# Optimization experiments

Measured on AMD Instinct MI355X. Metric: run time of the kernel, lower is better.

The kernel has to match this reference:

```python
import math
import jax, jax.numpy as jnp
import numpy as np

# ---------------- static structure (mirrors CG_woFilter_cuda + MyBatchNormWeightMM) ----------------
LMAX = 4
TAUS = [16, 16, 16, 16, 16]          # t_F: input channels per degree l
T_O  = [16, 16, 16, 16, 16]          # output channels per degree l after weight matmul
BN_EPS = 1e-5

# all (l, l1, l2) triples with l2 <= l1 <= lmax and |l1-l2| <= l <= min(l1+l2, lmax), sorted by (l,l1,l2)
TRIPLES = sorted([(l, l1, l2)
                  for l1 in range(LMAX + 1)
                  for l2 in range(l1 + 1)
                  for l in range(l1 - l2, min(l1 + l2, LMAX) + 1)])

T_FF = [0] * (LMAX + 1)              # t_FF[l] = sum over triples of taus[l1]*taus[l2]
for (l, l1, l2) in TRIPLES:
    T_FF[l] += TAUS[l1] * TAUS[l2]

def _cg_coef(j1, m1, j2, m2, j, m):
    """Clebsch-Gordan coefficient <j1 m1 j2 m2 | j m> (Condon-Shortley)."""
    if m1 + m2 != m:
        return 0.0
    f = math.factorial
    if j < abs(j1 - j2) or j > j1 + j2:
        return 0.0
    pref = math.sqrt((2 * j + 1) * f(j + j1 - j2) * f(j - j1 + j2) * f(j1 + j2 - j) / f(j1 + j2 + j + 1))
    pref *= math.sqrt(f(j + m) * f(j - m) * f(j1 - m1) * f(j1 + m1) * f(j2 - m2) * f(j2 + m2))
    s = 0.0
    for k in range(0, j1 + j2 - j + 1):
        if (j1 - m1 - k) < 0 or (j2 + m2 - k) < 0 or (j - j2 + m1 + k) < 0 or (j - j1 - m2 + k) < 0:
            continue
        s += ((-1.0) ** k) / (f(k) * f(j1 + j2 - j - k) * f(j1 - m1 - k)
                              * f(j2 + m2 - k) * f(j - j2 + m1 + k) * f(j - j1 - m2 + k))
    return pref * s

def _cg_matrix(l, l1, l2):
    C = np.zeros((2 * l + 1, 2 * l1 + 1, 2 * l2 + 1), dtype=np.float32)
    for m in range(-l, l + 1):
        for m1 in range(-l1, l1 + 1):
            m2 = m - m1
            if -l2 <= m2 <= l2:
                C[m + l, m1 + l1, m2 + l2] = _cg_coef(l1, m1, l2, m2, l, m)
    return C

CG_MATS = {t: jnp.asarray(_cg_matrix(*t)) for t in TRIPLES}

M_IN = sum(TAUS[l] * (2 * l + 1) for l in range(LMAX + 1))      # 400
W_LEN = sum(T_FF[l] * T_O[l] for l in range(LMAX + 1))          # 172032


def setup_inputs() -> dict:
    key = jax.random.key(0)
    k1, k2 = jax.random.split(key)
    B = 256
    Fs = jax.random.normal(k1, (B, M_IN, 2), dtype=jnp.float32)
    W = jax.random.normal(k2, (W_LEN, 2), dtype=jnp.float32) * 0.05
    return {"Fs": Fs, "W": W}


def reference(Fs, W):
    B = Fs.shape[0]
    # split input into per-degree blocks: F_l [B, tau, 2l+1, 2]
    Fl, off = [], 0
    for l in range(LMAX + 1):
        n = TAUS[l] * (2 * l + 1)
        Fl.append(Fs[:, off:off + n, :].reshape(B, TAUS[l], 2 * l + 1, 2))
        off += n
    # sparse CG tensor product: per-triple complex outer product contracted with CG coefs
    frags = [[] for _ in range(LMAX + 1)]
    for (l, l1, l2) in TRIPLES:
        C = CG_MATS[(l, l1, l2)]                     # [2l+1, 2l1+1, 2l2+1]
        a, b = Fl[l1], Fl[l2]
        ar, ai = a[..., 0], a[..., 1]
        br, bi = b[..., 0], b[..., 1]
        rr = jnp.einsum('bip,bjq,mpq->bijm', ar, br, C)
        ii = jnp.einsum('bip,bjq,mpq->bijm', ai, bi, C)
        ri = jnp.einsum('bip,bjq,mpq->bijm', ar, bi, C)
        ir = jnp.einsum('bip,bjq,mpq->bijm', ai, br, C)
        fr = (rr - ii).reshape(B, -1, 2 * l + 1)     # channels flattened as c1*tau2 + c2 (t_offsets order)
        fi = (ri + ir).reshape(B, -1, 2 * l + 1)
        frags[l].append(jnp.stack([fr, fi], axis=-1))
    # per-degree fragment batchnorm + complex weight matmul (FN_WMM)
    outs, woff = [], 0
    for l in range(LMAX + 1):
        FF = jnp.concatenate(frags[l], axis=1)       # [B, t_FF, 2l+1, 2]
        var = jnp.mean(jnp.sum(FF * FF, axis=-1), axis=(0, 2))      # per-channel mean |z|^2
        FFn = FF / (jnp.sqrt(var)[None, :, None, None] + BN_EPS)
        n = T_FF[l] * T_O[l]
        Wl = W[woff:woff + n].reshape(T_O[l], T_FF[l], 2)
        woff += n
        wr, wi = Wl[..., 0], Wl[..., 1]
        xr, xi = FFn[..., 0], FFn[..., 1]
        yr = jnp.einsum('oc,bcm->bom', wr, xr) - jnp.einsum('oc,bcm->bom', wi, xi)
        yi = jnp.einsum('oc,bcm->bom', wr, xi) + jnp.einsum('oc,bcm->bom', wi, xr)
        outs.append(jnp.stack([yr, yi], axis=-1).reshape(B, T_O[l] * (2 * l + 1), 2))
    return jnp.concatenate(outs, axis=1)             # [B, sum t_O[l]*(2l+1), 2] = [B, 400, 2]
```

## Files before the change

### kernel.cpp

```cpp
#include <hip/hip_runtime.h>
#include <math.h>

#define NTRI 42
#define NCH  10752
#define B_SZ 256
#define AH_PL 172032

typedef float    f32x4 __attribute__((ext_vector_type(4)));
typedef _Float16 half8 __attribute__((ext_vector_type(8)));
typedef _Float16 f16x2 __attribute__((ext_vector_type(2)));

constexpr int CT_L [NTRI]={0,0,0,0,0, 1,1,1,1,1,1,1,1, 2,2,2,2,2,2,2,2,2,2, 3,3,3,3,3,3,3,3,3,3, 4,4,4,4,4,4,4,4,4};
constexpr int CT_L1[NTRI]={0,1,2,3,4, 1,1,2,2,3,3,4,4, 1,2,2,2,3,3,3,4,4,4, 2,2,3,3,3,3,4,4,4,4, 2,3,3,3,4,4,4,4,4};
constexpr int CT_L2[NTRI]={0,1,2,3,4, 0,1,1,2,2,3,3,4, 1,0,1,2,1,2,3,2,3,4, 1,2,0,1,2,3,1,2,3,4, 2,1,2,3,0,1,2,3,4};
constexpr int CT_T [NTRI]={0,1,2,3,4, 0,1,2,3,4,5,6,7, 0,1,2,3,4,5,6,7,8,9, 0,1,2,3,4,5,6,7,8,9, 0,1,2,3,4,5,6,7,8};

constexpr int KL_t[5]    ={1280,2048,2560,2560,2304};
constexpr int GBASE_t[5] ={0,1280,3328,5888,8448};
constexpr int ROFF_t[5]  ={0,16,64,144,256};
constexpr int NM_t[5]    ={1,3,5,7,9};
constexpr int FFB_t[5]   ={0,327680,1900544,5177344,9764864};
#define FF_TOT 15073280
constexpr int PL_t[5]    ={0,5,29,79,149};
#define PART_PL 4096
#define PART_TOT (230*PART_PL)

__device__ const int   dCTL[NTRI]={0,0,0,0,0, 1,1,1,1,1,1,1,1, 2,2,2,2,2,2,2,2,2,2, 3,3,3,3,3,3,3,3,3,3, 4,4,4,4,4,4,4,4,4};
__device__ const int   dCTT[NTRI]={0,1,2,3,4, 0,1,2,3,4,5,6,7, 0,1,2,3,4,5,6,7,8,9, 0,1,2,3,4,5,6,7,8,9, 0,1,2,3,4,5,6,7,8};
__device__ const int   dK[5]   ={1280,2048,2560,2560,2304};
__device__ const int   dWOFF[5]={0,20480,53248,94208,135168};
__device__ const int   dNM[5]  ={1,3,5,7,9};
__device__ const int   dFFB[5] ={0,327680,1900544,5177344,9764864};
__device__ const int   dPL[5]  ={0,5,29,79,149};
__device__ const int   dGB[5]  ={0,1280,3328,5888,8448};
__device__ const int   dROFF[5]={0,16,64,144,256};
__device__ const int   dNT[5]  ={5,8,10,10,9};
__device__ const float dINV[5] ={1.f/256.f,1.f/768.f,1.f/1280.f,1.f/1792.f,1.f/2304.f};

__device__ float  g_vpart[64*NCH];
__device__ __align__(16) f16x2  g_ff[FF_TOT];
__device__ __align__(16) f16x2  g_ah[2*AH_PL];
__device__ float2 g_part[PART_TOT];

constexpr double cfact(int n){ double r=1.0; for(int i=2;i<=n;i++) r*=(double)i; return r; }
constexpr double csqrt_(double v){ double x = v>1.0? v:1.0; for(int i=0;i<80;i++) x = 0.5*(x+v/x); return x; }
constexpr double ccg(int j1,int m1,int j2,int m2,int j,int m){
    if(m1+m2!=m) return 0.0;
    double pref = csqrt_((2.0*j+1.0)*cfact(j+j1-j2)*cfact(j-j1+j2)*cfact(j1+j2-j)/cfact(j1+j2+j+1));
    pref *= csqrt_(cfact(j+m)*cfact(j-m)*cfact(j1-m1)*cfact(j1+m1)*cfact(j2-m2)*cfact(j2+m2));
    double s=0.0;
    for(int k=0;k<=j1+j2-j;k++){
        int a=j1-m1-k, bb=j2+m2-k, c=j-j2+m1+k, d=j-j1-m2+k;
        if(a<0||bb<0||c<0||d<0) continue;
        double term = 1.0/(cfact(k)*cfact(j1+j2-j-k)*cfact(a)*cfact(bb)*cfact(c)*cfact(d));
        s += (k&1)? -term : term;
    }
    return pref*s;
}
struct CG81 { float a[81]; };
constexpr CG81 makecg(int l,int l1,int l2){
    CG81 t{};
    const int n1=2*l1+1;
    for(int mi=0;mi<2*l+1;mi++)
        for(int p=0;p<n1;p++){
            const int m=mi-l, m1=p-l1, m2=m-m1;
            if(m2>=-l2 && m2<=l2) t.a[mi*n1+p]=(float)ccg(l1,m1,l2,m2,l,m);
        }
    return t;
}
template<int TR> struct CGC { static constexpr CG81 t = makecg(CT_L[TR],CT_L1[TR],CT_L2[TR]); };

template<int TR>
__device__ __forceinline__ void cg_compute_lds(const float2* __restrict__ sF,
                                               int i, int j, float2* __restrict__ ff){
    constexpr int L=CT_L[TR], L1=CT_L1[TR], L2=CT_L2[TR];
    constexpr int N1=2*L1+1, N2=2*L2+1, NM=2*L+1;
    float2 A[N1], Bv[N2];
    #pragma unroll
    for(int p=0;p<N1;p++) A[p]=sF[ROFF_t[L1]+i*N1+p];
    #pragma unroll
    for(int q=0;q<N2;q++) Bv[q]=sF[ROFF_t[L2]+j*N2+q];
    #pragma unroll
    for(int mi=0;mi<NM;mi++){
        float aR=0.f, aI=0.f;
        const int pLo = (mi-L+L1-L2) > 0 ? (mi-L+L1-L2) : 0;
        const int pHi = (mi-L+L1+L2) < 2*L1 ? (mi-L+L1+L2) : 2*L1;
        #pragma unroll
        for(int p=0;p<N1;p++){
            if(p>=pLo && p<=pHi){
                const float c = CGC<TR>::t.a[mi*N1+p];
                if(c != 0.f){
                    const int q = mi - L - p + L1 + L2;
                    const float2 a=A[p], b=Bv[q];
                    aR = fmaf(c, a.x*b.x - a.y*b.y, aR);
                    aI = fmaf(c, a.x*b.y + a.y*b.x, aI);
                }
            }
        }
        ff[mi]=make_float2(aR,aI);
    }
}

template<int TR>
__device__ __forceinline__ void cg_one(const float2* __restrict__ sF, int bc, int t){
    constexpr int L=CT_L[TR], NM=2*L+1, T=CT_T[TR], K=KL_t[L];
    constexpr int NMK=NM*K;
    const int i=t>>4, j=t&15;
    float n2=0.f;
    #pragma unroll
    for(int b4=0;b4<4;b4++){
        const int b=bc*4+b4;
        float2 ff[NM];
        cg_compute_lds<TR>(sF + b4*400, i, j, ff);
        const int base = FFB_t[L] + b*NMK + T*256 + t;
        #pragma unroll
        for(int m=0;m<NM;m++){
            n2 = fmaf(ff[m].x,ff[m].x,n2);
            n2 = fmaf(ff[m].y,ff[m].y,n2);
            f16x2 h; h.x=(_Float16)ff[m].x; h.y=(_Float16)ff[m].y;
            g_ff[base + m*K] = h;
        }
    }
    g_vpart[bc*NCH + GBASE_t[L] + T*256 + t] = n2;
}

template<int TR>
__device__ __forceinline__ void cg_disp(int tr, const float2* sF, int bc, int t){
    if constexpr (TR < NTRI){
        if(tr==TR) cg_one<TR>(sF,bc,t);
        else       cg_disp<TR+1>(tr,sF,bc,t);
    }
}

__global__ void __launch_bounds__(256) k_cg(const float2* __restrict__ Fs){
    __shared__ float4 sF4[800];
    const int bc=blockIdx.y, t=threadIdx.x;
    const float4* __restrict__ F4 = reinterpret_cast<const float4*>(Fs) + bc*800;
    sF4[t]      = F4[t];
    sF4[t+256]  = F4[t+256];
    sF4[t+512]  = F4[t+512];
    if(t<32) sF4[t+768] = F4[t+768];
    __syncthreads();
    cg_disp<0>(blockIdx.x, reinterpret_cast<const float2*>(sF4), bc, t);
}

__global__ void __launch_bounds__(256) k_wn(const float2* __restrict__ W2){
    const int tr=blockIdx.x, t=threadIdx.x;
    const int l=dCTL[tr], T=dCTT[tr], K=dK[l];
    const int ch = dGB[l] + T*256 + t;
    float s=0.f;
    #pragma unroll 8
    for(int bc=0;bc<64;bc++) s += g_vpart[bc*NCH + ch];
    const float invv = 1.f/(sqrtf(s*dINV[l])+1e-5f);
    const int base = dWOFF[l] + T*256 + t;
    #pragma unroll 4
    for(int o=0;o<16;o++){
        const float2 w = W2[base + o*K];
        f16x2 hr, hi;
        hr.x=(_Float16)( w.x*invv); hr.y=(_Float16)(-w.y*invv);
        hi.x=(_Float16)( w.y*invv); hi.y=(_Float16)( w.x*invv);
        g_ah[base + o*K]         = hr;
        g_ah[AH_PL + base + o*K] = hi;
    }
}

__global__ void __launch_bounds__(256) k_mm(){
    const int j=blockIdx.x;
    const int wv=threadIdx.x>>6, lane=threadIdx.x&63;
    const int bg=blockIdx.y*4+wv;
    const int l=(j<5)?0:(j<29)?1:(j<79)?2:(j<149)?3:4;
    const int nm=dNM[l];
    const int loc=j-dPL[l];
    const int T=loc/nm, m=loc-T*nm;
    const int K=dK[l];
    const int l15=lane&15, kg=lane>>4;
    const half8* __restrict__ Arp = reinterpret_cast<const half8*>(g_ah + dWOFF[l] + l15*K + T*256 + kg*4);
    const half8* __restrict__ Aip = reinterpret_cast<const half8*>(g_ah + AH_PL + dWOFF[l] + l15*K + T*256 + kg*4);
    const half8* __restrict__ Xp  = reinterpret_cast<const half8*>(g_ff + dFFB[l] + (bg*16+l15)*(nm*K) + m*K + T*256 + kg*4);
    f32x4 ar0={0.f,0.f,0.f,0.f}, ar1={0.f,0.f,0.f,0.f};
    f32x4 ai0={0.f,0.f,0.f,0.f}, ai1={0.f,0.f,0.f,0.f};
    #pragma unroll
    for(int ks=0; ks<16; ks++){
        const half8 Ar = Arp[ks*4];
        const half8 Ai = Aip[ks*4];
        const half8 Bf = Xp [ks*4];
        if(ks & 1){
            ar1 = __builtin_amdgcn_mfma_f32_16x16x32_f16(Ar, Bf, ar1, 0,0,0);
            ai1 = __builtin_amdgcn_mfma_f32_16x16x32_f16(Ai, Bf, ai1, 0,0,0);
        } else {
            ar0 = __builtin_amdgcn_mfma_f32_16x16x32_f16(Ar, Bf, ar0, 0,0,0);
            ai0 = __builtin_amdgcn_mfma_f32_16x16x32_f16(Ai, Bf, ai0, 0,0,0);
        }
    }
    const f32x4 ar = ar0 + ar1, ai = ai0 + ai1;
    float2* __restrict__ pp = g_part + j*PART_PL + bg*256;
    #pragma unroll
    for(int r=0;r<4;r++){
        pp[(kg*4+r)*16 + l15] = make_float2(ar[r], ai[r]);
    }
}

__global__ void __launch_bounds__(448) k_red(float2* __restrict__ out){
    const int b=blockIdx.x, r=threadIdx.x;
    if(r>=400) return;
    const int l = (r<16)?0:(r<64)?1:(r<144)?2:(r<256)?3:4;
    const int om = r - dROFF[l];
    const int nm = dNM[l];
    const int o = om/nm, m = om - o*nm;
    const float2* __restrict__ pp = g_part + (dPL[l]+m)*PART_PL + (b>>4)*256 + o*16 + (b&15);
    float2 s=make_float2(0.f,0.f);
    const int nt=dNT[l];
    for(int T=0;T<nt;T++){
        const float2 v = pp[T*nm*PART_PL];
        s.x+=v.x; s.y+=v.y;
    }
    out[b*400+r]=s;
}

extern "C" void kernel_launch(void* const* d_in, const int* in_sizes, int n_in,
                              void* d_out, int out_size, void* d_ws, size_t ws_size,
                              hipStream_t stream){
    const float2* Fs = (const float2*)d_in[0];
    const float2* W  = (const float2*)d_in[1];
    float2* out = (float2*)d_out;

    k_cg <<<dim3(NTRI,64), 256, 0, stream>>>(Fs);
    k_wn <<<dim3(NTRI),    256, 0, stream>>>(W);
    k_mm <<<dim3(230,4),   256, 0, stream>>>();
    k_red<<<dim3(B_SZ),    448, 0, stream>>>(out);
}
```

Before: 120.8 us.

## Pair channels per thread in CG, atomically reduce variance, double batch tiles in MFMA

The CG kernel now has each thread compute two adjacent output channels, sharing the A operand, and write them with a single half4 store. Each block handles 8 batch samples instead of 4, which halves the grid. Per-channel variance partials are accumulated with atomicAdd into one buffer that is zeroed by a memset, replacing the 64-way partial array and the reduction loop in k_wn. The matmul kernel gives each wave two batch tiles so the weight fragments are reused across four MFMAs, halving its grid. The trade-offs are an extra memset launch, atomic contention, and less parallelism per launch.

```diff
diff --git a/kernel.cpp b/kernel.cpp
--- a/kernel.cpp
+++ b/kernel.cpp
@@ -8,6 +8,7 @@
 
 typedef float    f32x4 __attribute__((ext_vector_type(4)));
 typedef _Float16 half8 __attribute__((ext_vector_type(8)));
+typedef _Float16 half4 __attribute__((ext_vector_type(4)));
 typedef _Float16 f16x2 __attribute__((ext_vector_type(2)));
 
 constexpr int CT_L [NTRI]={0,0,0,0,0, 1,1,1,1,1,1,1,1, 2,2,2,2,2,2,2,2,2,2, 3,3,3,3,3,3,3,3,3,3, 4,4,4,4,4,4,4,4,4};
@@ -37,7 +38,7 @@
 __device__ const int   dNT[5]  ={5,8,10,10,9};
 __device__ const float dINV[5] ={1.f/256.f,1.f/768.f,1.f/1280.f,1.f/1792.f,1.f/2304.f};
 
-__device__ float  g_vpart[64*NCH];
+__device__ float  g_varsum[NCH];
 __device__ __align__(16) f16x2  g_ff[FF_TOT];
 __device__ __align__(16) f16x2  g_ah[2*AH_PL];
 __device__ float2 g_part[PART_TOT];
@@ -71,18 +72,22 @@
 template<int TR> struct CGC { static constexpr CG81 t = makecg(CT_L[TR],CT_L1[TR],CT_L2[TR]); };
 
 template<int TR>
-__device__ __forceinline__ void cg_compute_lds(const float2* __restrict__ sF,
-                                               int i, int j, float2* __restrict__ ff){
+__device__ __forceinline__ void cg_pair(const float2* __restrict__ sF,
+                                        int i, int j0,
+                                        float2* __restrict__ ff0,
+                                        float2* __restrict__ ff1){
     constexpr int L=CT_L[TR], L1=CT_L1[TR], L2=CT_L2[TR];
     constexpr int N1=2*L1+1, N2=2*L2+1, NM=2*L+1;
-    float2 A[N1], Bv[N2];
+    float2 A[N1], B0[N2], B1[N2];
     #pragma unroll
     for(int p=0;p<N1;p++) A[p]=sF[ROFF_t[L1]+i*N1+p];
     #pragma unroll
-    for(int q=0;q<N2;q++) Bv[q]=sF[ROFF_t[L2]+j*N2+q];
+    for(int q=0;q<N2;q++) B0[q]=sF[ROFF_t[L2]+j0*N2+q];
+    #pragma unroll
+    for(int q=0;q<N2;q++) B1[q]=sF[ROFF_t[L2]+(j0+1)*N2+q];
     #pragma unroll
     for(int mi=0;mi<NM;mi++){
-        float aR=0.f, aI=0.f;
+        float aR0=0.f, aI0=0.f, aR1=0.f, aI1=0.f;
         const int pLo = (mi-L+L1-L2) > 0 ? (mi-L+L1-L2) : 0;
         const int pHi = (mi-L+L1+L2) < 2*L1 ? (mi-L+L1+L2) : 2*L1;
         #pragma unroll
@@ -91,66 +96,72 @@
                 const float c = CGC<TR>::t.a[mi*N1+p];
                 if(c != 0.f){
                     const int q = mi - L - p + L1 + L2;
-                    const float2 a=A[p], b=Bv[q];
-                    aR = fmaf(c, a.x*b.x - a.y*b.y, aR);
-                    aI = fmaf(c, a.x*b.y + a.y*b.x, aI);
+                    const float2 a=A[p];
+                    const float2 b0=B0[q], b1=B1[q];
+                    aR0 = fmaf(c, a.x*b0.x - a.y*b0.y, aR0);
+                    aI0 = fmaf(c, a.x*b0.y + a.y*b0.x, aI0);
+                    aR1 = fmaf(c, a.x*b1.x - a.y*b1.y, aR1);
+                    aI1 = fmaf(c, a.x*b1.y + a.y*b1.x, aI1);
                 }
             }
         }
-        ff[mi]=make_float2(aR,aI);
+        ff0[mi]=make_float2(aR0,aI0);
+        ff1[mi]=make_float2(aR1,aI1);
     }
 }
 
 template<int TR>
-__device__ __forceinline__ void cg_one(const float2* __restrict__ sF, int bc, int t){
+__device__ __forceinline__ void cg_one(const float2* __restrict__ sF, int bq, int t){
     constexpr int L=CT_L[TR], NM=2*L+1, T=CT_T[TR], K=KL_t[L];
     constexpr int NMK=NM*K;
-    const int i=t>>4, j=t&15;
-    float n2=0.f;
+    const int half = t>>7, tt = t&127;
+    const int ch0 = tt*2;
+    const int i = ch0>>4, j0 = ch0&15;
+    float n20=0.f, n21=0.f;
     #pragma unroll
     for(int b4=0;b4<4;b4++){
-        const int b=bc*4+b4;
-        float2 ff[NM];
-        cg_compute_lds<TR>(sF + b4*400, i, j, ff);
-        const int base = FFB_t[L] + b*NMK + T*256 + t;
+        const int slab = half*4+b4;
+        const int b = bq*8 + slab;
+        float2 ff0[NM], ff1[NM];
+        cg_pair<TR>(sF + slab*400, i, j0, ff0, ff1);
+        const int base = FFB_t[L] + b*NMK + T*256 + ch0;
         #pragma unroll
         for(int m=0;m<NM;m++){
-            n2 = fmaf(ff[m].x,ff[m].x,n2);
-            n2 = fmaf(ff[m].y,ff[m].y,n2);
-            f16x2 h; h.x=(_Float16)ff[m].x; h.y=(_Float16)ff[m].y;
-            g_ff[base + m*K] = h;
+            n20 = fmaf(ff0[m].x,ff0[m].x,n20); n20 = fmaf(ff0[m].y,ff0[m].y,n20);
+            n21 = fmaf(ff1[m].x,ff1[m].x,n21); n21 = fmaf(ff1[m].y,ff1[m].y,n21);
+            half4 h;
+            h[0]=(_Float16)ff0[m].x; h[1]=(_Float16)ff0[m].y;
+            h[2]=(_Float16)ff1[m].x; h[3]=(_Float16)ff1[m].y;
+            *reinterpret_cast<half4*>(g_ff + base + m*K) = h;
         }
     }
-    g_vpart[bc*NCH + GBASE_t[L] + T*256 + t] = n2;
+    atomicAdd(&g_varsum[GBASE_t[L] + T*256 + ch0    ], n20);
+    atomicAdd(&g_varsum[GBASE_t[L] + T*256 + ch0 + 1], n21);
 }
 
 template<int TR>
-__device__ __forceinline__ void cg_disp(int tr, const float2* sF, int bc, int t){
+__device__ __forceinline__ void cg_disp(int tr, const float2* sF, int bq, int t){
     if constexpr (TR < NTRI){
-        if(tr==TR) cg_one<TR>(sF,bc,t);
-        else       cg_disp<TR+1>(tr,sF,bc,t);
+        if(tr==TR) cg_one<TR>(sF,bq,t);
+        else       cg_disp<TR+1>(tr,sF,bq,t);
     }
 }
 
 __global__ void __launch_bounds__(256) k_cg(const float2* __restrict__ Fs){
-    __shared__ float4 sF4[800];
-    const int bc=blockIdx.y, t=threadIdx.x;
-    const float4* __restrict__ F4 = reinterpret_cast<const float4*>(Fs) + bc*800;
-    sF4[t]      = F4[t];
-    sF4[t+256]  = F4[t+256];
-    sF4[t+512]  = F4[t+512];
-    if(t<32) sF4[t+768] = F4[t+768];
+    __shared__ float4 sF4[1600];
+    const int bq=blockIdx.y, t=threadIdx.x;
+    const float4* __restrict__ F4 = reinterpret_cast<const float4*>(Fs) + bq*1600;
+    #pragma unroll
+    for(int k=0;k<6;k++) sF4[t + k*256] = F4[t + k*256];
+    if(t<64) sF4[t+1536] = F4[t+1536];
     __syncthreads();
-    cg_disp<0>(blockIdx.x, reinterpret_cast<const float2*>(sF4), bc, t);
+    cg_disp<0>(blockIdx.x, reinterpret_cast<const float2*>(sF4), bq, t);
 }
 
 __global__ void __launch_bounds__(256) k_wn(const float2* __restrict__ W2){
     const int tr=blockIdx.x, t=threadIdx.x;
     const int l=dCTL[tr], T=dCTT[tr], K=dK[l];
-    const int ch = dGB[l] + T*256 + t;
-    float s=0.f;
-    #pragma unroll 8
-    for(int bc=0;bc<64;bc++) s += g_vpart[bc*NCH + ch];
+    const float s = g_varsum[dGB[l] + T*256 + t];
     const float invv = 1.f/(sqrtf(s*dINV[l])+1e-5f);
     const int base = dWOFF[l] + T*256 + t;
     #pragma unroll 4
@@ -167,7 +178,8 @@
 __global__ void __launch_bounds__(256) k_mm(){
     const int j=blockIdx.x;
     const int wv=threadIdx.x>>6, lane=threadIdx.x&63;
-    const int bg=blockIdx.y*4+wv;
+    const int slot=blockIdx.y*4+wv;
+    const int bgA=slot, bgB=slot+8;
     const int l=(j<5)?0:(j<29)?1:(j<79)?2:(j<149)?3:4;
     const int nm=dNM[l];
     const int loc=j-dPL[l];
@@ -176,27 +188,27 @@
     const int l15=lane&15, kg=lane>>4;
     const half8* __restrict__ Arp = reinterpret_cast<const half8*>(g_ah + dWOFF[l] + l15*K + T*256 + kg*4);
     const half8* __restrict__ Aip = reinterpret_cast<const half8*>(g_ah + AH_PL + dWOFF[l] + l15*K + T*256 + kg*4);
-    const half8* __restrict__ Xp  = reinterpret_cast<const half8*>(g_ff + dFFB[l] + (bg*16+l15)*(nm*K) + m*K + T*256 + kg*4);
-    f32x4 ar0={0.f,0.f,0.f,0.f}, ar1={0.f,0.f,0.f,0.f};
-    f32x4 ai0={0.f,0.f,0.f,0.f}, ai1={0.f,0.f,0.f,0.f};
+    const half8* __restrict__ XpA = reinterpret_cast<const half8*>(g_ff + dFFB[l] + (bgA*16+l15)*(nm*K) + m*K + T*256 + kg*4);
+    const half8* __restrict__ XpB = reinterpret_cast<const half8*>(g_ff + dFFB[l] + (bgB*16+l15)*(nm*K) + m*K + T*256 + kg*4);
+    f32x4 arA={0.f,0.f,0.f,0.f}, aiA={0.f,0.f,0.f,0.f};
+    f32x4 arB={0.f,0.f,0.f,0.f}, aiB={0.f,0.f,0.f,0.f};
     #pragma unroll
     for(int ks=0; ks<16; ks++){
         const half8 Ar = Arp[ks*4];
         const half8 Ai = Aip[ks*4];
-        const half8 Bf = Xp [ks*4];
-        if(ks & 1){
-            ar1 = __builtin_amdgcn_mfma_f32_16x16x32_f16(Ar, Bf, ar1, 0,0,0);
-            ai1 = __builtin_amdgcn_mfma_f32_16x16x32_f16(Ai, Bf, ai1, 0,0,0);
-        } else {
-            ar0 = __builtin_amdgcn_mfma_f32_16x16x32_f16(Ar, Bf, ar0, 0,0,0);
-            ai0 = __builtin_amdgcn_mfma_f32_16x16x32_f16(Ai, Bf, ai0, 0,0,0);
-        }
-    }
-    const f32x4 ar = ar0 + ar1, ai = ai0 + ai1;
-    float2* __restrict__ pp = g_part + j*PART_PL + bg*256;
+        const half8 BA = XpA[ks*4];
+        const half8 BB = XpB[ks*4];
+        arA = __builtin_amdgcn_mfma_f32_16x16x32_f16(Ar, BA, arA, 0,0,0);
+        aiA = __builtin_amdgcn_mfma_f32_16x16x32_f16(Ai, BA, aiA, 0,0,0);
+        arB = __builtin_amdgcn_mfma_f32_16x16x32_f16(Ar, BB, arB, 0,0,0);
+        aiB = __builtin_amdgcn_mfma_f32_16x16x32_f16(Ai, BB, aiB, 0,0,0);
+    }
+    float2* __restrict__ ppA = g_part + j*PART_PL + bgA*256;
+    float2* __restrict__ ppB = g_part + j*PART_PL + bgB*256;
     #pragma unroll
     for(int r=0;r<4;r++){
-        pp[(kg*4+r)*16 + l15] = make_float2(ar[r], ai[r]);
+        ppA[(kg*4+r)*16 + l15] = make_float2(arA[r], aiA[r]);
+        ppB[(kg*4+r)*16 + l15] = make_float2(arB[r], aiB[r]);
     }
 }
 
@@ -224,8 +236,12 @@
     const float2* W  = (const float2*)d_in[1];
     float2* out = (float2*)d_out;
 
-    k_cg <<<dim3(NTRI,64), 256, 0, stream>>>(Fs);
+    void* dvs=nullptr;
+    hipGetSymbolAddress(&dvs, HIP_SYMBOL(g_varsum));
+    hipMemsetAsync(dvs, 0, NCH*sizeof(float), stream);
+
+    k_cg <<<dim3(NTRI,32), 256, 0, stream>>>(Fs);
     k_wn <<<dim3(NTRI),    256, 0, stream>>>(W);
-    k_mm <<<dim3(230,4),   256, 0, stream>>>();
+    k_mm <<<dim3(230,2),   256, 0, stream>>>();
     k_red<<<dim3(B_SZ),    448, 0, stream>>>(out);
 }
```

Result: faster. 116.5 us (-3.6%).
